# Kernel tuning notes

Hardware: AMD Instinct MI355X
Metric: run time of the kernel (lower is better)

## Reference

```python
import jax, jax.numpy as jnp
import numpy as np

MARGIN = 0.3

def setup_inputs() -> dict:
    key = jax.random.key(0)
    k1, k2 = jax.random.split(key)
    embeddings = jax.random.normal(k1, (8192, 512), dtype=jnp.float32)
    labels = jax.random.randint(k2, (8192,), 0, 128, dtype=jnp.int64)
    return {"embeddings": embeddings, "labels": labels}

def _pairwise_euclidean(x):
    # ||xi - xj|| via GEMM, matching torch reference (relu clamp + sqrt(.+1e-16))
    dot = x @ x.T                      # [B, B]
    sq = jnp.diagonal(dot)             # [B]
    d2 = sq[None, :] - 2.0 * dot + sq[:, None]
    d2 = jnp.maximum(d2, 0.0)
    return jnp.sqrt(d2 + 1e-16)

def reference(embeddings, labels):
    n = embeddings.shape[0]
    d = _pairwise_euclidean(embeddings)                 # [B, B]
    same = labels[:, None] == labels[None, :]           # [B, B]
    eye = jnp.eye(n, dtype=bool)
    mask_pos = same & ~eye
    mask_neg = ~same
    # fused masked row-wise reductions (hard mining)
    hardest_pos = jnp.max(jnp.where(mask_pos, d, -jnp.inf), axis=1)  # [B]
    hardest_neg = jnp.min(jnp.where(mask_neg, d, jnp.inf), axis=1)   # [B]
    valid = mask_pos.any(axis=1) & mask_neg.any(axis=1)              # [B]
    per_row = jax.nn.relu(hardest_pos - hardest_neg + MARGIN)
    per_row = jnp.where(valid, per_row, 0.0)
    denom = jnp.maximum(jnp.sum(valid.astype(per_row.dtype)), 1.0)
    return jnp.sum(per_row) / denom
```

## Files before the change

kernel.cpp:

```cpp
#include <hip/hip_runtime.h>

#define BATCH 8192
#define DIM   512

typedef __attribute__((ext_vector_type(4))) float  f32x4;
typedef __attribute__((ext_vector_type(8))) __bf16 bf16x8;

__device__ __forceinline__ unsigned short f2bf(float x) {
  unsigned u = __float_as_uint(x);
  u = (u + 0x7FFFu + ((u >> 16) & 1u)) >> 16;
  return (unsigned short)u;
}

__device__ __forceinline__ void load_lds16(const void* g, void* l) {
  __builtin_amdgcn_global_load_lds(
      (__attribute__((address_space(1))) void*)(g),
      (__attribute__((address_space(3))) void*)(l), 16, 0, 0);
}

__global__ __launch_bounds__(256) void prep_kernel(
    const float* __restrict__ X, unsigned short* __restrict__ Xb,
    float* __restrict__ sq, float* __restrict__ ctrl) {
  if (blockIdx.x == 0 && threadIdx.x == 0) {
    ctrl[0] = 0.f; ctrl[1] = 0.f;
    ((unsigned*)ctrl)[2] = 0u;
  }
  int wave = threadIdx.x >> 6, lane = threadIdx.x & 63;
  int row = blockIdx.x * 4 + wave;
  const float4* xr = (const float4*)(X + (size_t)row * DIM);
  float4 a = xr[lane * 2];
  float4 b = xr[lane * 2 + 1];
  float s = a.x*a.x + a.y*a.y + a.z*a.z + a.w*a.w
          + b.x*b.x + b.y*b.y + b.z*b.z + b.w*b.w;
  uint4 p;
  p.x = (unsigned)f2bf(a.x) | ((unsigned)f2bf(a.y) << 16);
  p.y = (unsigned)f2bf(a.z) | ((unsigned)f2bf(a.w) << 16);
  p.z = (unsigned)f2bf(b.x) | ((unsigned)f2bf(b.y) << 16);
  p.w = (unsigned)f2bf(b.z) | ((unsigned)f2bf(b.w) << 16);
  ((uint4*)(Xb + (size_t)row * DIM))[lane] = p;
  #pragma unroll
  for (int off = 32; off > 0; off >>= 1) s += __shfl_down(s, off);
  if (lane == 0) sq[row] = s;
}

template<bool DIAG>
__device__ __forceinline__ void tile_epilogue(
    const f32x4 (&acc)[4][8],
    const float* __restrict__ sqj_s, const int* __restrict__ labj_s,
    const int* __restrict__ labi_s,
    int j0loc, int wn, int wm, int lc, int quad, int i0, int jbase,
    float (&rpos)[16], float (&rneg)[16]) {
  float sqj_r[8]; int labj_r[8]; int jg_r[8];
  #pragma unroll
  for (int ni = 0; ni < 8; ni++) {
    int jj = j0loc + wn * 128 + ni * 16 + lc;
    sqj_r[ni]  = sqj_s[jj];
    labj_r[ni] = labj_s[jj];
    jg_r[ni]   = jbase + jj;
  }
  #pragma unroll
  for (int mi = 0; mi < 4; mi++) {
    #pragma unroll
    for (int r = 0; r < 4; r++) {
      int idx = mi * 4 + r;
      int li = labi_s[wm * 64 + mi * 16 + quad * 4 + r];
      int ii = i0 + wm * 64 + mi * 16 + quad * 4 + r;
      float rp = rpos[idx], rn = rneg[idx];
      #pragma unroll
      for (int ni = 0; ni < 8; ni++) {
        float v = fmaf(-2.f, acc[mi][ni][r], sqj_r[ni]);
        bool same = (li == labj_r[ni]);
        bool posok = DIAG ? (same && (jg_r[ni] != ii)) : same;
        rp = fmaxf(rp, posok ? v : -3e38f);
        rn = fminf(rn, same ? 3e38f : v);
      }
      rpos[idx] = rp; rneg[idx] = rn;
    }
  }
}

__global__ __launch_bounds__(256, 2) void triplet_mfma(
    const unsigned short* __restrict__ Xb, const float* __restrict__ sq,
    const int* __restrict__ labels,
    float* __restrict__ pos_part, float* __restrict__ neg_part) {
  __shared__ __align__(16) unsigned short Asm[128 * 64];
  __shared__ __align__(16) unsigned short Bsm[256 * 64];
  __shared__ float sqj_s[1024];
  __shared__ int   labj_s[1024];
  __shared__ int   labi_s[128];

  int tid = threadIdx.x;
  int bid = blockIdx.x;
  int It = bid & 63, jc = bid >> 6;
  int i0 = It * 128, jbase = jc * 1024;

  for (int t = tid; t < 1024; t += 256) {
    sqj_s[t]  = sq[jbase + t];
    labj_s[t] = labels[jbase + t];
  }
  if (tid < 128) labi_s[tid] = labels[i0 + tid];
  __syncthreads();

  int wave = tid >> 6, lane = tid & 63;
  int wm = wave >> 1, wn = wave & 1;
  int quad = lane >> 4, lc = lane & 15;

  float rpos[16], rneg[16];
  #pragma unroll
  for (int t = 0; t < 16; t++) { rpos[t] = -3e38f; rneg[t] = 3e38f; }

  int rc = lane >> 3;
  int gcol = ((lane & 7) ^ rc) * 8;

  for (int js = 0; js < 4; js++) {
    int j0loc = js * 256;
    f32x4 acc[4][8];
    #pragma unroll
    for (int mi = 0; mi < 4; mi++)
      #pragma unroll
      for (int ni = 0; ni < 8; ni++)
        acc[mi][ni] = (f32x4){0.f, 0.f, 0.f, 0.f};

    for (int k0 = 0; k0 < DIM; k0 += 64) {
      #pragma unroll
      for (int t = 0; t < 4; t++) {
        int c = wave * 4 + t;
        int row = c * 8 + rc;
        load_lds16(Xb + (size_t)(i0 + row) * DIM + k0 + gcol, &Asm[c * 512]);
      }
      #pragma unroll
      for (int t = 0; t < 8; t++) {
        int c = wave * 8 + t;
        int row = c * 8 + rc;
        load_lds16(Xb + (size_t)(jbase + j0loc + row) * DIM + k0 + gcol, &Bsm[c * 512]);
      }
      __syncthreads();
      #pragma unroll
      for (int kk = 0; kk < 64; kk += 32) {
        int kc = kk >> 3;
        int asel = ((kc + quad) ^ (lc & 7)) * 8;
        bf16x8 af[4], bfr[8];
        #pragma unroll
        for (int mi = 0; mi < 4; mi++)
          af[mi] = *(const bf16x8*)&Asm[(wm * 64 + mi * 16 + lc) * 64 + asel];
        #pragma unroll
        for (int ni = 0; ni < 8; ni++)
          bfr[ni] = *(const bf16x8*)&Bsm[(wn * 128 + ni * 16 + lc) * 64 + asel];
        #pragma unroll
        for (int mi = 0; mi < 4; mi++)
          #pragma unroll
          for (int ni = 0; ni < 8; ni++)
            acc[mi][ni] = __builtin_amdgcn_mfma_f32_16x16x32_bf16(
                af[mi], bfr[ni], acc[mi][ni], 0, 0, 0);
      }
      __syncthreads();
    }

    int ilo = i0 + wm * 64, jlo = jbase + j0loc + wn * 128;
    bool has_diag = (ilo < jlo + 128) && (jlo < ilo + 64);
    if (has_diag)
      tile_epilogue<true >(acc, sqj_s, labj_s, labi_s, j0loc, wn, wm, lc, quad, i0, jbase, rpos, rneg);
    else
      tile_epilogue<false>(acc, sqj_s, labj_s, labi_s, j0loc, wn, wm, lc, quad, i0, jbase, rpos, rneg);
  }

  #pragma unroll
  for (int m = 1; m <= 8; m <<= 1) {
    #pragma unroll
    for (int t = 0; t < 16; t++) {
      rpos[t] = fmaxf(rpos[t], __shfl_xor(rpos[t], m));
      rneg[t] = fminf(rneg[t], __shfl_xor(rneg[t], m));
    }
  }

  if (lc == 0) {
    int slot = jc * 2 + wn;
    #pragma unroll
    for (int mi = 0; mi < 4; mi++)
      #pragma unroll
      for (int r = 0; r < 4; r++) {
        int row = i0 + wm * 64 + mi * 16 + quad * 4 + r;
        pos_part[slot * BATCH + row] = rpos[mi * 4 + r];
        neg_part[slot * BATCH + row] = rneg[mi * 4 + r];
      }
  }
}

__global__ __launch_bounds__(256) void final_kernel(
    const float* __restrict__ pos_part, const float* __restrict__ neg_part,
    const float* __restrict__ sq, float* __restrict__ ctrl,
    float* __restrict__ out) {
  int i = blockIdx.x * 256 + threadIdx.x;
  float p = -3e38f, n = 3e38f;
  #pragma unroll
  for (int s = 0; s < 16; s++) {
    p = fmaxf(p, pos_part[s * BATCH + i]);
    n = fminf(n, neg_part[s * BATCH + i]);
  }
  float term = 0.f, cnt = 0.f;
  if (p > -1e37f && n < 1e37f) {
    float si = sq[i];
    float dp = sqrtf(fmaxf(si + p, 0.f) + 1e-16f);
    float dn = sqrtf(fmaxf(si + n, 0.f) + 1e-16f);
    term = fmaxf(dp - dn + 0.3f, 0.f);
    cnt = 1.f;
  }
  #pragma unroll
  for (int off = 32; off > 0; off >>= 1) {
    term += __shfl_down(term, off);
    cnt  += __shfl_down(cnt, off);
  }
  __shared__ float ss[4], sc[4];
  int wave = threadIdx.x >> 6, lane = threadIdx.x & 63;
  if (lane == 0) { ss[wave] = term; sc[wave] = cnt; }
  __syncthreads();
  if (threadIdx.x == 0) {
    atomicAdd(&ctrl[0], ss[0] + ss[1] + ss[2] + ss[3]);
    atomicAdd(&ctrl[1], sc[0] + sc[1] + sc[2] + sc[3]);
    __threadfence();
    unsigned t = atomicAdd((unsigned*)&ctrl[2], 1u);
    if (t == 31u) {
      float S = atomicAdd(&ctrl[0], 0.f);
      float C = atomicAdd(&ctrl[1], 0.f);
      out[0] = S / fmaxf(C, 1.f);
    }
  }
}

extern "C" void kernel_launch(void* const* d_in, const int* in_sizes, int n_in,
                              void* d_out, int out_size, void* d_ws, size_t ws_size,
                              hipStream_t stream) {
  const float* X      = (const float*)d_in[0];
  const int*   labels = (const int*)d_in[1];
  float* out = (float*)d_out;
  char* ws = (char*)d_ws;

  unsigned short* Xb  = (unsigned short*)ws;
  float*    sq        = (float*)(ws + (8u << 20));
  float*    ctrl      = (float*)(ws + (8u << 20) + (32u << 10));
  float*    pos_part  = (float*)(ws + (8u << 20) + (64u << 10));
  float*    neg_part  = (float*)(ws + (8u << 20) + (64u << 10) + (512u << 10));

  prep_kernel<<<BATCH / 4, 256, 0, stream>>>(X, Xb, sq, ctrl);
  triplet_mfma<<<512, 256, 0, stream>>>(Xb, sq, labels, pos_part, neg_part);
  final_kernel<<<BATCH / 256, 256, 0, stream>>>(pos_part, neg_part, sq, ctrl, out);
}
```

Measured before the change: 145.1 us.

## Exploit distance-matrix symmetry to compute only upper-triangle tiles with dual row/column reductions

The Gram matrix is symmetric, so only diagonal-straddling and upper-triangle tiles are computed. Each off-diagonal tile reduces along both rows and columns, with the column side using sq[i] in place of sq[j]. That roughly halves the MFMA and load work. Partial results are stored as order-preserving encoded unsigned ints in larger partial buffers, cleared by memsets, and the final kernel reduces 96 slots instead of 16. The cost is a heavier epilogue, extra memsets, a serial loop that decodes tile indices, and more partial-buffer traffic.

```diff
diff --git a/kernel.cpp b/kernel.cpp
--- a/kernel.cpp
+++ b/kernel.cpp
@@ -16,6 +16,15 @@
   __builtin_amdgcn_global_load_lds(
       (__attribute__((address_space(1))) void*)(g),
       (__attribute__((address_space(3))) void*)(l), 16, 0, 0);
+}
+
+__device__ __forceinline__ unsigned enc(float f) {
+  unsigned u = __float_as_uint(f);
+  return u ^ (unsigned)(((int)u >> 31) | 0x80000000);
+}
+__device__ __forceinline__ float dec(unsigned k) {
+  unsigned u = (k & 0x80000000u) ? (k ^ 0x80000000u) : ~k;
+  return __uint_as_float(u);
 }
 
 __global__ __launch_bounds__(256) void prep_kernel(
@@ -43,38 +52,80 @@
   if (lane == 0) sq[row] = s;
 }
 
-template<bool DIAG>
-__device__ __forceinline__ void tile_epilogue(
-    const f32x4 (&acc)[4][8],
-    const float* __restrict__ sqj_s, const int* __restrict__ labj_s,
-    const int* __restrict__ labi_s,
-    int j0loc, int wn, int wm, int lc, int quad, int i0, int jbase,
-    float (&rpos)[16], float (&rneg)[16]) {
-  float sqj_r[8]; int labj_r[8]; int jg_r[8];
+template<bool STRAD>
+__device__ __forceinline__ void epilogue(
+    const f32x4 (&acc)[4][8], const float* __restrict__ sq,
+    const int* __restrict__ labels,
+    int i0, int jwin, int wm, int wn, int quad, int lc,
+    unsigned (*ibuf)[128][2], unsigned (*jbuf)[256][2]) {
+  float sqj_r[8]; int labj_r[8];
   #pragma unroll
   for (int ni = 0; ni < 8; ni++) {
-    int jj = j0loc + wn * 128 + ni * 16 + lc;
-    sqj_r[ni]  = sqj_s[jj];
-    labj_r[ni] = labj_s[jj];
-    jg_r[ni]   = jbase + jj;
-  }
+    int j = jwin + wn * 128 + ni * 16 + lc;
+    sqj_r[ni] = sq[j]; labj_r[ni] = labels[j];
+  }
+  float rpos[16], rneg[16];
+  float jp[8], jn[8];
+  #pragma unroll
+  for (int x = 0; x < 8; x++) { jp[x] = -3e38f; jn[x] = 3e38f; }
   #pragma unroll
   for (int mi = 0; mi < 4; mi++) {
     #pragma unroll
     for (int r = 0; r < 4; r++) {
-      int idx = mi * 4 + r;
-      int li = labi_s[wm * 64 + mi * 16 + quad * 4 + r];
-      int ii = i0 + wm * 64 + mi * 16 + quad * 4 + r;
-      float rp = rpos[idx], rn = rneg[idx];
+      int ig = i0 + wm * 64 + mi * 16 + quad * 4 + r;
+      int li = labels[ig];
+      float si = sq[ig];
+      float rp = -3e38f, rn = 3e38f;
       #pragma unroll
       for (int ni = 0; ni < 8; ni++) {
-        float v = fmaf(-2.f, acc[mi][ni][r], sqj_r[ni]);
+        float a = acc[mi][ni][r];
+        float v = fmaf(-2.f, a, sqj_r[ni]);
         bool same = (li == labj_r[ni]);
-        bool posok = DIAG ? (same && (jg_r[ni] != ii)) : same;
+        bool posok = same;
+        if (STRAD) posok = same && ((jwin + wn * 128 + ni * 16 + lc) != ig);
         rp = fmaxf(rp, posok ? v : -3e38f);
         rn = fminf(rn, same ? 3e38f : v);
-      }
-      rpos[idx] = rp; rneg[idx] = rn;
+        if (!STRAD) {
+          float v2 = fmaf(-2.f, a, si);
+          jp[ni] = fmaxf(jp[ni], same ? v2 : -3e38f);
+          jn[ni] = fminf(jn[ni], same ? 3e38f : v2);
+        }
+      }
+      rpos[mi * 4 + r] = rp; rneg[mi * 4 + r] = rn;
+    }
+  }
+  #pragma unroll
+  for (int m = 1; m <= 8; m <<= 1)
+    #pragma unroll
+    for (int x = 0; x < 16; x++) {
+      rpos[x] = fmaxf(rpos[x], __shfl_xor(rpos[x], m));
+      rneg[x] = fminf(rneg[x], __shfl_xor(rneg[x], m));
+    }
+  if (lc == 0) {
+    #pragma unroll
+    for (int mi = 0; mi < 4; mi++)
+      #pragma unroll
+      for (int r = 0; r < 4; r++) {
+        int row = wm * 64 + mi * 16 + quad * 4 + r;
+        ibuf[wn][row][0] = enc(rpos[mi * 4 + r]);
+        ibuf[wn][row][1] = enc(rneg[mi * 4 + r]);
+      }
+  }
+  if (!STRAD) {
+    #pragma unroll
+    for (int m = 16; m <= 32; m <<= 1)
+      #pragma unroll
+      for (int x = 0; x < 8; x++) {
+        jp[x] = fmaxf(jp[x], __shfl_xor(jp[x], m));
+        jn[x] = fminf(jn[x], __shfl_xor(jn[x], m));
+      }
+    if (quad == 0) {
+      #pragma unroll
+      for (int ni = 0; ni < 8; ni++) {
+        int col = wn * 128 + ni * 16 + lc;
+        jbuf[wm][col][0] = enc(jp[ni]);
+        jbuf[wm][col][1] = enc(jn[ni]);
+      }
     }
   }
 }
@@ -82,38 +133,35 @@
 __global__ __launch_bounds__(256, 2) void triplet_mfma(
     const unsigned short* __restrict__ Xb, const float* __restrict__ sq,
     const int* __restrict__ labels,
-    float* __restrict__ pos_part, float* __restrict__ neg_part) {
+    unsigned* __restrict__ pos_i, unsigned* __restrict__ neg_i,
+    unsigned* __restrict__ pos_j, unsigned* __restrict__ neg_j) {
   __shared__ __align__(16) unsigned short Asm[128 * 64];
   __shared__ __align__(16) unsigned short Bsm[256 * 64];
-  __shared__ float sqj_s[1024];
-  __shared__ int   labj_s[1024];
-  __shared__ int   labi_s[128];
-
-  int tid = threadIdx.x;
-  int bid = blockIdx.x;
-  int It = bid & 63, jc = bid >> 6;
-  int i0 = It * 128, jbase = jc * 1024;
-
-  for (int t = tid; t < 1024; t += 256) {
-    sqj_s[t]  = sq[jbase + t];
-    labj_s[t] = labels[jbase + t];
-  }
-  if (tid < 128) labi_s[tid] = labels[i0 + tid];
-  __syncthreads();
-
+  __shared__ unsigned ibuf[2][128][2];
+  __shared__ unsigned jbuf[2][256][2];
+
+  int tid = threadIdx.x, bid = blockIdx.x;
   int wave = tid >> 6, lane = tid & 63;
   int wm = wave >> 1, wn = wave & 1;
   int quad = lane >> 4, lc = lane & 15;
-
-  float rpos[16], rneg[16];
-  #pragma unroll
-  for (int t = 0; t < 16; t++) { rpos[t] = -3e38f; rneg[t] = 3e38f; }
-
   int rc = lane >> 3;
   int gcol = ((lane & 7) ^ rc) * 8;
 
-  for (int js = 0; js < 4; js++) {
-    int j0loc = js * 256;
+  int start = (bid * 33) >> 4, end = ((bid + 1) * 33) >> 4;
+  for (int t = start; t < end; ++t) {
+    int It, Js; bool strad;
+    if (t < 64) { It = t; Js = t >> 1; strad = true; }
+    else {
+      int u = t - 64; It = 0; Js = 0;
+      for (int s = 0; s < 64; s++) {
+        int c = 31 - (s >> 1);
+        if (u < c) { It = s; Js = (s >> 1) + 1 + u; break; }
+        u -= c;
+      }
+      strad = false;
+    }
+    int i0 = It * 128, jwin = Js * 256;
+
     f32x4 acc[4][8];
     #pragma unroll
     for (int mi = 0; mi < 4; mi++)
@@ -123,16 +171,16 @@
 
     for (int k0 = 0; k0 < DIM; k0 += 64) {
       #pragma unroll
-      for (int t = 0; t < 4; t++) {
-        int c = wave * 4 + t;
+      for (int tt = 0; tt < 4; tt++) {
+        int c = wave * 4 + tt;
         int row = c * 8 + rc;
         load_lds16(Xb + (size_t)(i0 + row) * DIM + k0 + gcol, &Asm[c * 512]);
       }
       #pragma unroll
-      for (int t = 0; t < 8; t++) {
-        int c = wave * 8 + t;
+      for (int tt = 0; tt < 8; tt++) {
+        int c = wave * 8 + tt;
         int row = c * 8 + rc;
-        load_lds16(Xb + (size_t)(jbase + j0loc + row) * DIM + k0 + gcol, &Bsm[c * 512]);
+        load_lds16(Xb + (size_t)(jwin + row) * DIM + k0 + gcol, &Bsm[c * 512]);
       }
       __syncthreads();
       #pragma unroll
@@ -156,47 +204,45 @@
       __syncthreads();
     }
 
-    int ilo = i0 + wm * 64, jlo = jbase + j0loc + wn * 128;
-    bool has_diag = (ilo < jlo + 128) && (jlo < ilo + 64);
-    if (has_diag)
-      tile_epilogue<true >(acc, sqj_s, labj_s, labi_s, j0loc, wn, wm, lc, quad, i0, jbase, rpos, rneg);
+    if (strad)
+      epilogue<true >(acc, sq, labels, i0, jwin, wm, wn, quad, lc, ibuf, jbuf);
     else
-      tile_epilogue<false>(acc, sqj_s, labj_s, labi_s, j0loc, wn, wm, lc, quad, i0, jbase, rpos, rneg);
-  }
-
-  #pragma unroll
-  for (int m = 1; m <= 8; m <<= 1) {
-    #pragma unroll
-    for (int t = 0; t < 16; t++) {
-      rpos[t] = fmaxf(rpos[t], __shfl_xor(rpos[t], m));
-      rneg[t] = fminf(rneg[t], __shfl_xor(rneg[t], m));
-    }
-  }
-
-  if (lc == 0) {
-    int slot = jc * 2 + wn;
-    #pragma unroll
-    for (int mi = 0; mi < 4; mi++)
-      #pragma unroll
-      for (int r = 0; r < 4; r++) {
-        int row = i0 + wm * 64 + mi * 16 + quad * 4 + r;
-        pos_part[slot * BATCH + row] = rpos[mi * 4 + r];
-        neg_part[slot * BATCH + row] = rneg[mi * 4 + r];
-      }
+      epilogue<false>(acc, sq, labels, i0, jwin, wm, wn, quad, lc, ibuf, jbuf);
+    __syncthreads();
+
+    if (tid < 128) {
+      unsigned p = max(ibuf[0][tid][0], ibuf[1][tid][0]);
+      unsigned n = min(ibuf[0][tid][1], ibuf[1][tid][1]);
+      pos_i[(size_t)Js * BATCH + i0 + tid] = p;
+      neg_i[(size_t)Js * BATCH + i0 + tid] = n;
+    }
+    if (!strad) {
+      unsigned p = max(jbuf[0][tid][0], jbuf[1][tid][0]);
+      unsigned n = min(jbuf[0][tid][1], jbuf[1][tid][1]);
+      pos_j[(size_t)It * BATCH + jwin + tid] = p;
+      neg_j[(size_t)It * BATCH + jwin + tid] = n;
+    }
   }
 }
 
 __global__ __launch_bounds__(256) void final_kernel(
-    const float* __restrict__ pos_part, const float* __restrict__ neg_part,
+    const unsigned* __restrict__ pos_i, const unsigned* __restrict__ neg_i,
+    const unsigned* __restrict__ pos_j, const unsigned* __restrict__ neg_j,
     const float* __restrict__ sq, float* __restrict__ ctrl,
     float* __restrict__ out) {
   int i = blockIdx.x * 256 + threadIdx.x;
-  float p = -3e38f, n = 3e38f;
-  #pragma unroll
-  for (int s = 0; s < 16; s++) {
-    p = fmaxf(p, pos_part[s * BATCH + i]);
-    n = fminf(n, neg_part[s * BATCH + i]);
-  }
+  unsigned pe = 0u, ne = 0xFFFFFFFFu;
+  #pragma unroll 4
+  for (int s = 0; s < 32; s++) {
+    pe = max(pe, pos_i[(size_t)s * BATCH + i]);
+    ne = min(ne, neg_i[(size_t)s * BATCH + i]);
+  }
+  #pragma unroll 4
+  for (int s = 0; s < 64; s++) {
+    pe = max(pe, pos_j[(size_t)s * BATCH + i]);
+    ne = min(ne, neg_j[(size_t)s * BATCH + i]);
+  }
+  float p = dec(pe), n = dec(ne);
   float term = 0.f, cnt = 0.f;
   if (p > -1e37f && n < 1e37f) {
     float si = sq[i];
@@ -235,13 +281,20 @@
   float* out = (float*)d_out;
   char* ws = (char*)d_ws;
 
-  unsigned short* Xb  = (unsigned short*)ws;
-  float*    sq        = (float*)(ws + (8u << 20));
-  float*    ctrl      = (float*)(ws + (8u << 20) + (32u << 10));
-  float*    pos_part  = (float*)(ws + (8u << 20) + (64u << 10));
-  float*    neg_part  = (float*)(ws + (8u << 20) + (64u << 10) + (512u << 10));
-
+  const size_t SLOT = (size_t)BATCH * 4;
+  unsigned short* Xb = (unsigned short*)ws;
+  float* sq   = (float*)(ws + (8u << 20));
+  float* ctrl = (float*)(ws + (8u << 20) + (32u << 10));
+  char*  posb = ws + (8u << 20) + (64u << 10);
+  char*  negb = posb + 96 * SLOT;
+  unsigned* pos_i = (unsigned*)posb;
+  unsigned* pos_j = (unsigned*)(posb + 32 * SLOT);
+  unsigned* neg_i = (unsigned*)negb;
+  unsigned* neg_j = (unsigned*)(negb + 32 * SLOT);
+
+  hipMemsetAsync(posb, 0x00, 96 * SLOT, stream);
+  hipMemsetAsync(negb, 0xFF, 96 * SLOT, stream);
   prep_kernel<<<BATCH / 4, 256, 0, stream>>>(X, Xb, sq, ctrl);
-  triplet_mfma<<<512, 256, 0, stream>>>(Xb, sq, labels, pos_part, neg_part);
-  final_kernel<<<BATCH / 256, 256, 0, stream>>>(pos_part, neg_part, sq, ctrl, out);
-}
+  triplet_mfma<<<512, 256, 0, stream>>>(Xb, sq, labels, pos_i, neg_i, pos_j, neg_j);
+  final_kernel<<<BATCH / 256, 256, 0, stream>>>(pos_i, neg_i, pos_j, neg_j, sq, ctrl, out);
+}
```

New measurement: 148.7 us. 2.5% more time.
